# Kernel tuning notes

Hardware: AMD Instinct MI355X
Metric: run time of the kernel (lower is better)

The kernel has to match this reference:

```python
import jax, jax.numpy as jnp
import numpy as np

N_NODES = 100000
N_EDGES = 1600000
IN_DIM, HID_DIM, OUT_DIM = 128, 128, 64


def setup_inputs() -> dict:
    key = jax.random.key(0)
    k1, k2, k3, k4 = jax.random.split(key, 4)
    x = jax.random.normal(k1, (N_NODES, IN_DIM), dtype=jnp.float32)
    edge_index = jax.random.randint(k2, (2, N_EDGES), 0, N_NODES, dtype=jnp.int64)
    W1 = jax.random.normal(k3, (IN_DIM, HID_DIM), dtype=jnp.float32) * (1.0 / np.sqrt(IN_DIM))
    b1 = jnp.zeros((HID_DIM,), dtype=jnp.float32)
    W2 = jax.random.normal(k4, (HID_DIM, OUT_DIM), dtype=jnp.float32) * (1.0 / np.sqrt(HID_DIM))
    b2 = jnp.zeros((OUT_DIM,), dtype=jnp.float32)
    return {"x": x, "edge_index": edge_index, "W1": W1, "b1": b1, "W2": W2, "b2": b2}


def _gcn_conv(x, W, b, src, dst, num_nodes):
    # PyG GCNConv (normalize=True): h = D^{-1/2} A_hat D^{-1/2} (x W) + b
    h = x @ W  # [N, out]
    ones = jnp.ones(src.shape[0], dtype=h.dtype)
    deg = jax.ops.segment_sum(ones, dst, num_segments=num_nodes)  # in-degree incl self-loops
    dinv = jnp.where(deg > 0, jax.lax.rsqrt(deg), jnp.zeros_like(deg))
    norm = dinv[src] * dinv[dst]  # [E]
    msg = h[src] * norm[:, None]  # gather + scale, [E, out]
    out = jax.ops.segment_sum(msg, dst, num_segments=num_nodes)  # scatter-add
    return out + b


def reference(x, edge_index, W1, b1, W2, b2):
    n = x.shape[0]
    loop = jnp.arange(n, dtype=edge_index.dtype)
    src = jnp.concatenate([edge_index[0], loop])  # add_self_loops=True
    dst = jnp.concatenate([edge_index[1], loop])
    h = jax.nn.elu(_gcn_conv(x, W1, b1, src, dst, n))
    out = jax.nn.elu(_gcn_conv(h, W2, b2, src, dst, n))
    return out
```

## Files before the change

kernel.cpp:

```cpp
#include <hip/hip_runtime.h>
#include <hip/hip_bf16.h>

#define N_NODES 100000
#define N_EDGES 1600000
#define IN_DIM  128
#define HID_DIM 128
#define OUT_DIM 64

#define BKT_BITS 9
#define BKT_SIZE 512
#define NBUCK    ((N_NODES + BKT_SIZE - 1) / BKT_SIZE)
#define BCAP     8768
#define EPB      2048
#define CAST_BLKS 3125

typedef __attribute__((ext_vector_type(8))) short short8;
typedef __attribute__((ext_vector_type(4))) float floatx4;

__device__ __forceinline__ float eluf(float x) { return x > 0.0f ? x : expm1f(x); }
__device__ __forceinline__ unsigned short bfbits(float f) {
    union { __hip_bfloat16 h; unsigned short u; } c; c.h = __float2bfloat16(f); return c.u;
}
__device__ __forceinline__ unsigned packbf(float a, float b) {
    return (unsigned)bfbits(a) | ((unsigned)bfbits(b) << 16);
}
__device__ __forceinline__ float lo16(unsigned u) { return __uint_as_float(u << 16); }
__device__ __forceinline__ float hi16(unsigned u) { return __uint_as_float(u & 0xffff0000u); }

__device__ __forceinline__ int esrc(const int* ei, int e, int is64) {
    return is64 ? ei[2 * e] : ei[e];
}
__device__ __forceinline__ int edst(const int* ei, int e, int is64) {
    return is64 ? ei[2 * (N_EDGES + e)] : ei[N_EDGES + e];
}

__global__ void k_init(const int* __restrict__ ei, int* __restrict__ flag,
                       int* __restrict__ cursor) {
    __shared__ int acc;
    if (threadIdx.x == 0) acc = 0;
    __syncthreads();
    int v = 0;
    for (int e = threadIdx.x; e < 1024; e += 256) v |= ei[2 * e + 1];
    atomicOr(&acc, v);
    __syncthreads();
    if (threadIdx.x == 0) flag[0] = (acc == 0) ? 1 : 0;
    if (threadIdx.x < NBUCK) cursor[threadIdx.x] = 0;
}

__launch_bounds__(256)
__global__ void k_bucket(const int* __restrict__ ei, const int* __restrict__ flag,
                         int* __restrict__ cursor, unsigned* __restrict__ eb) {
    __shared__ int hist[NBUCK];
    __shared__ int base[NBUCK];
    int t = threadIdx.x;
    int is64 = flag[0];
    int e0 = blockIdx.x * EPB;
    int s[8], d[8];
#pragma unroll
    for (int q = 0; q < 8; q++) {
        int e = e0 + q * 256 + t;
        if (e < N_EDGES) { s[q] = esrc(ei, e, is64); d[q] = edst(ei, e, is64); }
        else d[q] = -1;
    }
    for (int i = t; i < NBUCK; i += 256) hist[i] = 0;
    __syncthreads();
#pragma unroll
    for (int q = 0; q < 8; q++)
        if (d[q] >= 0) atomicAdd(&hist[d[q] >> BKT_BITS], 1);
    __syncthreads();
    for (int i = t; i < NBUCK; i += 256) {
        int h = hist[i];
        base[i] = (h > 0) ? atomicAdd(&cursor[i], h) : 0;
    }
    __syncthreads();
#pragma unroll
    for (int q = 0; q < 8; q++)
        if (d[q] >= 0) {
            int bk = d[q] >> BKT_BITS;
            int p = atomicAdd(&base[bk], 1);
            if (p < BCAP)
                eb[bk * BCAP + p] = ((unsigned)s[q] << BKT_BITS) | (unsigned)(d[q] & (BKT_SIZE - 1));
        }
}

__launch_bounds__(256)
__global__ void k_csr_cast(const int* __restrict__ cursor, unsigned* __restrict__ eb,
                           unsigned short* __restrict__ row16, unsigned char* __restrict__ deg8,
                           float* __restrict__ dinv,
                           const float4* __restrict__ x4, uint2* __restrict__ xb) {
    __shared__ unsigned stage[BCAP];
    __shared__ int hist[BKT_SIZE];
    __shared__ int excl[BKT_SIZE];
    __shared__ int cur[BKT_SIZE];
    __shared__ int sc[256];
    int t = threadIdx.x, b = blockIdx.x;
    if (b >= NBUCK) {
        int i0 = (b - NBUCK) * 1024 + t;
#pragma unroll
        for (int q = 0; q < 4; q++) {
            int i = i0 + q * 256;
            if (i < N_NODES * (IN_DIM / 4)) {
                float4 v = x4[i];
                uint2 o = { packbf(v.x, v.y), packbf(v.z, v.w) };
                xb[i] = o;
            }
        }
        return;
    }
    int cbeg = b * BCAP;
    int count = cursor[b];
    if (count > BCAP) count = BCAP;
    for (int i = t; i < BKT_SIZE; i += 256) hist[i] = 0;
    __syncthreads();
    for (int i = t; i < count; i += 256) {
        unsigned e = eb[cbeg + i];
        stage[i] = e;
        atomicAdd(&hist[e & (BKT_SIZE - 1)], 1);
    }
    __syncthreads();
    int h0 = hist[2 * t], h1 = hist[2 * t + 1];
    int s = h0 + h1;
    sc[t] = s;
    __syncthreads();
    int acc = s;
    for (int off = 1; off < 256; off <<= 1) {
        int v = (t >= off) ? sc[t - off] : 0;
        __syncthreads();
        acc += v; sc[t] = acc;
        __syncthreads();
    }
    int ex = acc - s;
    excl[2 * t] = ex;       excl[2 * t + 1] = ex + h0;
    cur[2 * t] = ex;        cur[2 * t + 1] = ex + h0;
    int nbase = b * BKT_SIZE;
    for (int i = t; i < BKT_SIZE; i += 256) {
        int n = nbase + i;
        if (n < N_NODES) {
            row16[n] = (unsigned short)excl[i];
            deg8[n] = (unsigned char)hist[i];
            dinv[n] = rsqrtf((float)hist[i] + 1.0f);
        }
    }
    __syncthreads();
    for (int i = t; i < count; i += 256) {
        unsigned e = stage[i];
        int p = atomicAdd(&cur[e & (BKT_SIZE - 1)], 1);
        eb[cbeg + p] = e >> BKT_BITS;
    }
}

__launch_bounds__(256)
__global__ void k_gather1(const uint2* __restrict__ xb2, const float* __restrict__ dinv,
                          const unsigned short* __restrict__ row16,
                          const unsigned char* __restrict__ deg8,
                          const unsigned* __restrict__ csr, uint2* __restrict__ agg2) {
    int w = (blockIdx.x * blockDim.x + threadIdx.x) >> 5;
    int p = threadIdx.x & 31;
    if (w >= N_NODES) return;
    int beg = (w >> BKT_BITS) * BCAP + row16[w];
    int end = beg + deg8[w];
    float dd = dinv[w];
    uint2 sv = xb2[w * 32 + p];
    float a0 = lo16(sv.x) * dd, a1 = hi16(sv.x) * dd;
    float a2 = lo16(sv.y) * dd, a3 = hi16(sv.y) * dd;
    int j = beg;
    for (; j + 8 <= end; j += 8) {
        int s[8]; float wd[8]; uint2 u[8];
#pragma unroll
        for (int q = 0; q < 8; q++) s[q] = (int)csr[j + q];
#pragma unroll
        for (int q = 0; q < 8; q++) wd[q] = dinv[s[q]];
#pragma unroll
        for (int q = 0; q < 8; q++) u[q] = xb2[s[q] * 32 + p];
#pragma unroll
        for (int q = 0; q < 8; q++) {
            a0 += lo16(u[q].x) * wd[q]; a1 += hi16(u[q].x) * wd[q];
            a2 += lo16(u[q].y) * wd[q]; a3 += hi16(u[q].y) * wd[q];
        }
    }
    for (; j + 2 <= end; j += 2) {
        int s0 = (int)csr[j], s1 = (int)csr[j + 1];
        float w0 = dinv[s0], w1 = dinv[s1];
        uint2 u0 = xb2[s0 * 32 + p];
        uint2 u1 = xb2[s1 * 32 + p];
        a0 += lo16(u0.x) * w0 + lo16(u1.x) * w1; a1 += hi16(u0.x) * w0 + hi16(u1.x) * w1;
        a2 += lo16(u0.y) * w0 + lo16(u1.y) * w1; a3 += hi16(u0.y) * w0 + hi16(u1.y) * w1;
    }
    if (j < end) {
        int s0 = (int)csr[j]; float w0 = dinv[s0];
        uint2 u0 = xb2[s0 * 32 + p];
        a0 += lo16(u0.x) * w0; a1 += hi16(u0.x) * w0;
        a2 += lo16(u0.y) * w0; a3 += hi16(u0.y) * w0;
    }
    uint2 o = { packbf(a0 * dd, a1 * dd), packbf(a2 * dd, a3 * dd) };
    agg2[w * 32 + p] = o;
}

__launch_bounds__(256)
__global__ void k_gather2(const uint2* __restrict__ h2, const float* __restrict__ dinv,
                          const unsigned short* __restrict__ row16,
                          const unsigned char* __restrict__ deg8,
                          const unsigned* __restrict__ csr,
                          const float* __restrict__ b2, float4* __restrict__ out) {
    int w = (blockIdx.x * blockDim.x + threadIdx.x) >> 4;
    int p = threadIdx.x & 15;
    if (w >= N_NODES) return;
    float4 bias = *(const float4*)(b2 + 4 * p);
    int beg = (w >> BKT_BITS) * BCAP + row16[w];
    int end = beg + deg8[w];
    float dd = dinv[w];
    uint2 sv = h2[w * 16 + p];
    float a0 = lo16(sv.x) * dd, a1 = hi16(sv.x) * dd;
    float a2 = lo16(sv.y) * dd, a3 = hi16(sv.y) * dd;
    int j = beg;
    for (; j + 8 <= end; j += 8) {
        int s[8]; float wd[8]; uint2 u[8];
#pragma unroll
        for (int q = 0; q < 8; q++) s[q] = (int)csr[j + q];
#pragma unroll
        for (int q = 0; q < 8; q++) wd[q] = dinv[s[q]];
#pragma unroll
        for (int q = 0; q < 8; q++) u[q] = h2[s[q] * 16 + p];
#pragma unroll
        for (int q = 0; q < 8; q++) {
            a0 += lo16(u[q].x) * wd[q]; a1 += hi16(u[q].x) * wd[q];
            a2 += lo16(u[q].y) * wd[q]; a3 += hi16(u[q].y) * wd[q];
        }
    }
    for (; j + 2 <= end; j += 2) {
        int s0 = (int)csr[j], s1 = (int)csr[j + 1];
        float w0 = dinv[s0], w1 = dinv[s1];
        uint2 u0 = h2[s0 * 16 + p];
        uint2 u1 = h2[s1 * 16 + p];
        a0 += lo16(u0.x) * w0 + lo16(u1.x) * w1; a1 += hi16(u0.x) * w0 + hi16(u1.x) * w1;
        a2 += lo16(u0.y) * w0 + lo16(u1.y) * w1; a3 += hi16(u0.y) * w0 + hi16(u1.y) * w1;
    }
    if (j < end) {
        int s0 = (int)csr[j]; float w0 = dinv[s0];
        uint2 u0 = h2[s0 * 16 + p];
        a0 += lo16(u0.x) * w0; a1 += hi16(u0.x) * w0;
        a2 += lo16(u0.y) * w0; a3 += hi16(u0.y) * w0;
    }
    a0 *= dd; a1 *= dd; a2 *= dd; a3 *= dd;
    float4 r = { eluf(a0 + bias.x), eluf(a1 + bias.y), eluf(a2 + bias.z), eluf(a3 + bias.w) };
    out[w * 16 + p] = r;
}

__launch_bounds__(256)
__global__ void k_gemm1_mfma(unsigned* __restrict__ agg, const float* __restrict__ W1,
                             const float* __restrict__ b1, int nblk) {
    __shared__ short w1p[4][8][64][8];
    int t = threadIdx.x;
    for (int idx = t; idx < 8192; idx += 256) {
        int j2 = idx & 3, l = (idx >> 2) & 63, ct = (idx >> 8) & 7, kk = idx >> 11;
        int k = kk * 32 + (l >> 4) * 8 + j2 * 2;
        int c = ct * 16 + (l & 15);
        ((unsigned*)w1p)[idx] = packbf(W1[k * HID_DIM + c], W1[(k + 1) * HID_DIM + c]);
    }
    int lane = t & 63, wave = t >> 6;
    int q = lane >> 4, m = lane & 15;
    floatx4 bias[8];
#pragma unroll
    for (int ct = 0; ct < 8; ct++) bias[ct] = *(const floatx4*)(b1 + ct * 16 + q * 4);
    __syncthreads();
    for (int blk = blockIdx.x * 4 + wave; blk < nblk; blk += gridDim.x * 4) {
        int r = blk * 16 + m;
        const short8* arow = (const short8*)(agg + r * 64);
        short8 bfr[4];
#pragma unroll
        for (int kk = 0; kk < 4; kk++) bfr[kk] = arow[kk * 4 + q];
        floatx4 acc[8];
#pragma unroll
        for (int ct = 0; ct < 8; ct++) acc[ct] = (floatx4)0.0f;
#pragma unroll
        for (int kk = 0; kk < 4; kk++)
#pragma unroll
            for (int ct = 0; ct < 8; ct++) {
                short8 af = *(const short8*)(&w1p[kk][ct][lane][0]);
                acc[ct] = __builtin_amdgcn_mfma_f32_16x16x32_bf16(af, bfr[kk], acc[ct], 0, 0, 0);
            }
        unsigned* hrow = agg + r * 64;
#pragma unroll
        for (int ct = 0; ct < 8; ct++) {
            uint2 o;
            o.x = packbf(eluf(acc[ct][0] + bias[ct][0]), eluf(acc[ct][1] + bias[ct][1]));
            o.y = packbf(eluf(acc[ct][2] + bias[ct][2]), eluf(acc[ct][3] + bias[ct][3]));
            *(uint2*)(hrow + ct * 8 + q * 2) = o;
        }
    }
}

__launch_bounds__(256)
__global__ void k_gemm2_mfma(const unsigned* __restrict__ h1, const float* __restrict__ W2,
                             unsigned* __restrict__ h2, int nblk) {
    __shared__ short w2p[4][4][64][8];
    int t = threadIdx.x;
    for (int idx = t; idx < 4096; idx += 256) {
        int j2 = idx & 3, l = (idx >> 2) & 63, ct = (idx >> 8) & 3, kk = idx >> 10;
        int k = kk * 32 + (l >> 4) * 8 + j2 * 2;
        int c = ct * 16 + (l & 15);
        ((unsigned*)w2p)[idx] = packbf(W2[k * OUT_DIM + c], W2[(k + 1) * OUT_DIM + c]);
    }
    int lane = t & 63, wave = t >> 6;
    int q = lane >> 4, m = lane & 15;
    __syncthreads();
    for (int blk = blockIdx.x * 4 + wave; blk < nblk; blk += gridDim.x * 4) {
        int r = blk * 16 + m;
        const short8* arow = (const short8*)(h1 + r * 64);
        short8 bfr[4];
#pragma unroll
        for (int kk = 0; kk < 4; kk++) bfr[kk] = arow[kk * 4 + q];
        floatx4 acc[4];
#pragma unroll
        for (int ct = 0; ct < 4; ct++) acc[ct] = (floatx4)0.0f;
#pragma unroll
        for (int kk = 0; kk < 4; kk++)
#pragma unroll
            for (int ct = 0; ct < 4; ct++) {
                short8 af = *(const short8*)(&w2p[kk][ct][lane][0]);
                acc[ct] = __builtin_amdgcn_mfma_f32_16x16x32_bf16(af, bfr[kk], acc[ct], 0, 0, 0);
            }
        unsigned* orow = h2 + r * 32;
#pragma unroll
        for (int ct = 0; ct < 4; ct++) {
            uint2 o;
            o.x = packbf(acc[ct][0], acc[ct][1]);
            o.y = packbf(acc[ct][2], acc[ct][3]);
            *(uint2*)(orow + ct * 8 + q * 2) = o;
        }
    }
}

extern "C" void kernel_launch(void* const* d_in, const int* in_sizes, int n_in,
                              void* d_out, int out_size, void* d_ws, size_t ws_size,
                              hipStream_t stream) {
    const float* x  = (const float*)d_in[0];
    const int*   ei = (const int*)d_in[1];
    const float* W1 = (const float*)d_in[2];
    const float* b1 = (const float*)d_in[3];
    const float* W2 = (const float*)d_in[4];
    const float* b2 = (const float*)d_in[5];

    const size_t OFF_FLAG  = 0;
    const size_t OFF_CUR   = 16;
    const size_t OFF_ROW16 = 272;
    const size_t OFF_DEG8  = 50272;
    const size_t OFF_DINV  = 75272;
    const size_t OFF_EB    = 175272;
    const size_t OFF_XB    = 1893800;
    const size_t OFF_AGG   = 8293800;
    const size_t needed = (OFF_AGG + 6400000) * 4;
    if (ws_size < needed) return;

    int*            flag   = (int*)d_ws + OFF_FLAG;
    int*            cursor = (int*)d_ws + OFF_CUR;
    unsigned short* row16  = (unsigned short*)((int*)d_ws + OFF_ROW16);
    unsigned char*  deg8   = (unsigned char*)((int*)d_ws + OFF_DEG8);
    float*          dinv   = (float*)d_ws + OFF_DINV;
    unsigned*       eb     = (unsigned*)d_ws + OFF_EB;
    unsigned*       xb     = (unsigned*)d_ws + OFF_XB;
    unsigned*       agg    = (unsigned*)d_ws + OFF_AGG;

    k_init<<<1, 256, 0, stream>>>(ei, flag, cursor);
    k_bucket<<<(N_EDGES + EPB - 1) / EPB, 256, 0, stream>>>(ei, flag, cursor, eb);
    k_csr_cast<<<NBUCK + CAST_BLKS, 256, 0, stream>>>(cursor, eb, row16, deg8, dinv,
                                                      (const float4*)x, (uint2*)xb);

    k_gather1<<<(N_NODES * 32 + 255) / 256, 256, 0, stream>>>(
        (const uint2*)xb, dinv, row16, deg8, eb, (uint2*)agg);
    k_gemm1_mfma<<<1024, 256, 0, stream>>>(agg, W1, b1, N_NODES / 16);

    k_gemm2_mfma<<<1024, 256, 0, stream>>>(agg, W2, xb, N_NODES / 16);
    k_gather2<<<(N_NODES * 16 + 255) / 256, 256, 0, stream>>>(
        (const uint2*)xb, dinv, row16, deg8, eb, b2, (float4*)d_out);
}
```

Before: 326.9 us.

## Pre-scale features by dinv, tile-sort CSR neighbors, widen gathers to full wave

Source rows are multiplied by dinv once, in a separate cast kernel for layer 1 and in the GEMM2 epilogue for layer 2. This removes the per-edge dinv lookup and multiply from both gathers. The CSR build now sorts each node's neighbors by source tile (8 tiles), which should make gathered rows more local in cache. Both gathers use one 64-lane wave per node with readfirstlane bounds, and layer 2 splits edges across two half-waves combined with a shuffle. In exchange, the input cast is no longer fused into the CSR kernel, so it runs as an extra serialized launch, and CSR binning uses more shared memory.

```diff
diff --git a/kernel.cpp b/kernel.cpp
--- a/kernel.cpp
+++ b/kernel.cpp
@@ -12,7 +12,7 @@
 #define NBUCK    ((N_NODES + BKT_SIZE - 1) / BKT_SIZE)
 #define BCAP     8768
 #define EPB      2048
-#define CAST_BLKS 3125
+#define NTILE    8
 
 typedef __attribute__((ext_vector_type(8))) short short8;
 typedef __attribute__((ext_vector_type(4))) float floatx4;
@@ -26,6 +26,7 @@
 }
 __device__ __forceinline__ float lo16(unsigned u) { return __uint_as_float(u << 16); }
 __device__ __forceinline__ float hi16(unsigned u) { return __uint_as_float(u & 0xffff0000u); }
+__device__ __forceinline__ unsigned tile_of(unsigned src) { return (src * 8u) / 100000u; }
 
 __device__ __forceinline__ int esrc(const int* ei, int e, int is64) {
     return is64 ? ei[2 * e] : ei[e];
@@ -84,42 +85,29 @@
 }
 
 __launch_bounds__(256)
-__global__ void k_csr_cast(const int* __restrict__ cursor, unsigned* __restrict__ eb,
-                           unsigned short* __restrict__ row16, unsigned char* __restrict__ deg8,
-                           float* __restrict__ dinv,
-                           const float4* __restrict__ x4, uint2* __restrict__ xb) {
+__global__ void k_csr(const int* __restrict__ cursor, unsigned* __restrict__ eb,
+                      unsigned short* __restrict__ row16, unsigned char* __restrict__ deg8,
+                      float* __restrict__ dinv) {
     __shared__ unsigned stage[BCAP];
-    __shared__ int hist[BKT_SIZE];
-    __shared__ int excl[BKT_SIZE];
-    __shared__ int cur[BKT_SIZE];
+    __shared__ int bins[BKT_SIZE * NTILE];
     __shared__ int sc[256];
     int t = threadIdx.x, b = blockIdx.x;
-    if (b >= NBUCK) {
-        int i0 = (b - NBUCK) * 1024 + t;
-#pragma unroll
-        for (int q = 0; q < 4; q++) {
-            int i = i0 + q * 256;
-            if (i < N_NODES * (IN_DIM / 4)) {
-                float4 v = x4[i];
-                uint2 o = { packbf(v.x, v.y), packbf(v.z, v.w) };
-                xb[i] = o;
-            }
-        }
-        return;
-    }
     int cbeg = b * BCAP;
     int count = cursor[b];
     if (count > BCAP) count = BCAP;
-    for (int i = t; i < BKT_SIZE; i += 256) hist[i] = 0;
+    for (int i = t; i < BKT_SIZE * NTILE; i += 256) bins[i] = 0;
     __syncthreads();
     for (int i = t; i < count; i += 256) {
         unsigned e = eb[cbeg + i];
         stage[i] = e;
-        atomicAdd(&hist[e & (BKT_SIZE - 1)], 1);
-    }
-    __syncthreads();
-    int h0 = hist[2 * t], h1 = hist[2 * t + 1];
-    int s = h0 + h1;
+        unsigned key = ((e & (BKT_SIZE - 1)) << 3) + tile_of(e >> BKT_BITS);
+        atomicAdd(&bins[key], 1);
+    }
+    __syncthreads();
+    int loc[16];
+    int s = 0;
+#pragma unroll
+    for (int i = 0; i < 16; i++) { loc[i] = bins[t * 16 + i]; s += loc[i]; }
     sc[t] = s;
     __syncthreads();
     int acc = s;
@@ -129,121 +117,143 @@
         acc += v; sc[t] = acc;
         __syncthreads();
     }
-    int ex = acc - s;
-    excl[2 * t] = ex;       excl[2 * t + 1] = ex + h0;
-    cur[2 * t] = ex;        cur[2 * t + 1] = ex + h0;
+    int run = acc - s;
+#pragma unroll
+    for (int i = 0; i < 16; i++) { bins[t * 16 + i] = run; run += loc[i]; }
+    __syncthreads();
     int nbase = b * BKT_SIZE;
     for (int i = t; i < BKT_SIZE; i += 256) {
         int n = nbase + i;
         if (n < N_NODES) {
-            row16[n] = (unsigned short)excl[i];
-            deg8[n] = (unsigned char)hist[i];
-            dinv[n] = rsqrtf((float)hist[i] + 1.0f);
+            int st = bins[i << 3];
+            int en = (i == BKT_SIZE - 1) ? count : bins[(i + 1) << 3];
+            row16[n] = (unsigned short)st;
+            deg8[n] = (unsigned char)(en - st);
+            dinv[n] = rsqrtf((float)(en - st) + 1.0f);
         }
     }
     __syncthreads();
     for (int i = t; i < count; i += 256) {
         unsigned e = stage[i];
-        int p = atomicAdd(&cur[e & (BKT_SIZE - 1)], 1);
-        eb[cbeg + p] = e >> BKT_BITS;
-    }
-}
-
-__launch_bounds__(256)
-__global__ void k_gather1(const uint2* __restrict__ xb2, const float* __restrict__ dinv,
+        unsigned src = e >> BKT_BITS;
+        unsigned key = ((e & (BKT_SIZE - 1)) << 3) + tile_of(src);
+        int p = atomicAdd(&bins[key], 1);
+        eb[cbeg + p] = src;
+    }
+}
+
+__global__ void k_cast_scale(const float4* __restrict__ x4, const float* __restrict__ dinv,
+                             uint2* __restrict__ xbs) {
+    int i = blockIdx.x * blockDim.x + threadIdx.x;
+    if (i >= N_NODES * (IN_DIM / 4)) return;
+    float dd = dinv[i >> 5];
+    float4 v = x4[i];
+    uint2 o = { packbf(v.x * dd, v.y * dd), packbf(v.z * dd, v.w * dd) };
+    xbs[i] = o;
+}
+
+__launch_bounds__(256)
+__global__ void k_gather1(const unsigned* __restrict__ xbs, const float* __restrict__ dinv,
                           const unsigned short* __restrict__ row16,
                           const unsigned char* __restrict__ deg8,
-                          const unsigned* __restrict__ csr, uint2* __restrict__ agg2) {
-    int w = (blockIdx.x * blockDim.x + threadIdx.x) >> 5;
-    int p = threadIdx.x & 31;
+                          const unsigned* __restrict__ csr, unsigned* __restrict__ agg) {
+    int w = (blockIdx.x * blockDim.x + threadIdx.x) >> 6;
+    int lane = threadIdx.x & 63;
     if (w >= N_NODES) return;
     int beg = (w >> BKT_BITS) * BCAP + row16[w];
-    int end = beg + deg8[w];
+    int dg = deg8[w];
+    beg = __builtin_amdgcn_readfirstlane(beg);
+    int end = beg + __builtin_amdgcn_readfirstlane(dg);
     float dd = dinv[w];
-    uint2 sv = xb2[w * 32 + p];
-    float a0 = lo16(sv.x) * dd, a1 = hi16(sv.x) * dd;
-    float a2 = lo16(sv.y) * dd, a3 = hi16(sv.y) * dd;
+    unsigned sv = xbs[w * 64 + lane];
+    float a0 = lo16(sv), a1 = hi16(sv);
     int j = beg;
     for (; j + 8 <= end; j += 8) {
-        int s[8]; float wd[8]; uint2 u[8];
+        int s[8]; unsigned u[8];
 #pragma unroll
         for (int q = 0; q < 8; q++) s[q] = (int)csr[j + q];
 #pragma unroll
-        for (int q = 0; q < 8; q++) wd[q] = dinv[s[q]];
-#pragma unroll
-        for (int q = 0; q < 8; q++) u[q] = xb2[s[q] * 32 + p];
-#pragma unroll
-        for (int q = 0; q < 8; q++) {
-            a0 += lo16(u[q].x) * wd[q]; a1 += hi16(u[q].x) * wd[q];
-            a2 += lo16(u[q].y) * wd[q]; a3 += hi16(u[q].y) * wd[q];
-        }
-    }
-    for (; j + 2 <= end; j += 2) {
+        for (int q = 0; q < 8; q++) u[q] = xbs[s[q] * 64 + lane];
+#pragma unroll
+        for (int q = 0; q < 8; q++) { a0 += lo16(u[q]); a1 += hi16(u[q]); }
+    }
+    if (j + 4 <= end) {
+        int s[4]; unsigned u[4];
+#pragma unroll
+        for (int q = 0; q < 4; q++) s[q] = (int)csr[j + q];
+#pragma unroll
+        for (int q = 0; q < 4; q++) u[q] = xbs[s[q] * 64 + lane];
+#pragma unroll
+        for (int q = 0; q < 4; q++) { a0 += lo16(u[q]); a1 += hi16(u[q]); }
+        j += 4;
+    }
+    if (j + 2 <= end) {
         int s0 = (int)csr[j], s1 = (int)csr[j + 1];
-        float w0 = dinv[s0], w1 = dinv[s1];
-        uint2 u0 = xb2[s0 * 32 + p];
-        uint2 u1 = xb2[s1 * 32 + p];
-        a0 += lo16(u0.x) * w0 + lo16(u1.x) * w1; a1 += hi16(u0.x) * w0 + hi16(u1.x) * w1;
-        a2 += lo16(u0.y) * w0 + lo16(u1.y) * w1; a3 += hi16(u0.y) * w0 + hi16(u1.y) * w1;
+        unsigned u0 = xbs[s0 * 64 + lane], u1 = xbs[s1 * 64 + lane];
+        a0 += lo16(u0) + lo16(u1); a1 += hi16(u0) + hi16(u1);
+        j += 2;
     }
     if (j < end) {
-        int s0 = (int)csr[j]; float w0 = dinv[s0];
-        uint2 u0 = xb2[s0 * 32 + p];
-        a0 += lo16(u0.x) * w0; a1 += hi16(u0.x) * w0;
-        a2 += lo16(u0.y) * w0; a3 += hi16(u0.y) * w0;
-    }
-    uint2 o = { packbf(a0 * dd, a1 * dd), packbf(a2 * dd, a3 * dd) };
-    agg2[w * 32 + p] = o;
-}
-
-__launch_bounds__(256)
-__global__ void k_gather2(const uint2* __restrict__ h2, const float* __restrict__ dinv,
+        unsigned u0 = xbs[(int)csr[j] * 64 + lane];
+        a0 += lo16(u0); a1 += hi16(u0);
+    }
+    agg[w * 64 + lane] = packbf(a0 * dd, a1 * dd);
+}
+
+__launch_bounds__(256)
+__global__ void k_gather2(const unsigned* __restrict__ h2s, const float* __restrict__ dinv,
                           const unsigned short* __restrict__ row16,
                           const unsigned char* __restrict__ deg8,
                           const unsigned* __restrict__ csr,
-                          const float* __restrict__ b2, float4* __restrict__ out) {
-    int w = (blockIdx.x * blockDim.x + threadIdx.x) >> 4;
-    int p = threadIdx.x & 15;
+                          const float* __restrict__ b2, float2* __restrict__ out) {
+    int w = (blockIdx.x * blockDim.x + threadIdx.x) >> 6;
+    int lane = threadIdx.x & 63;
     if (w >= N_NODES) return;
-    float4 bias = *(const float4*)(b2 + 4 * p);
+    int half = lane >> 5, p = lane & 31;
     int beg = (w >> BKT_BITS) * BCAP + row16[w];
-    int end = beg + deg8[w];
+    int dg = deg8[w];
+    beg = __builtin_amdgcn_readfirstlane(beg);
+    int end = beg + __builtin_amdgcn_readfirstlane(dg);
     float dd = dinv[w];
-    uint2 sv = h2[w * 16 + p];
-    float a0 = lo16(sv.x) * dd, a1 = hi16(sv.x) * dd;
-    float a2 = lo16(sv.y) * dd, a3 = hi16(sv.y) * dd;
+    unsigned sv = h2s[w * 32 + p];
+    float a0 = half ? 0.0f : lo16(sv);
+    float a1 = half ? 0.0f : hi16(sv);
     int j = beg;
     for (; j + 8 <= end; j += 8) {
-        int s[8]; float wd[8]; uint2 u[8];
+        int s[8]; unsigned u[4];
 #pragma unroll
         for (int q = 0; q < 8; q++) s[q] = (int)csr[j + q];
 #pragma unroll
-        for (int q = 0; q < 8; q++) wd[q] = dinv[s[q]];
-#pragma unroll
-        for (int q = 0; q < 8; q++) u[q] = h2[s[q] * 16 + p];
-#pragma unroll
-        for (int q = 0; q < 8; q++) {
-            a0 += lo16(u[q].x) * wd[q]; a1 += hi16(u[q].x) * wd[q];
-            a2 += lo16(u[q].y) * wd[q]; a3 += hi16(u[q].y) * wd[q];
-        }
-    }
-    for (; j + 2 <= end; j += 2) {
+        for (int i = 0; i < 4; i++) u[i] = h2s[s[2 * i + half] * 32 + p];
+#pragma unroll
+        for (int i = 0; i < 4; i++) { a0 += lo16(u[i]); a1 += hi16(u[i]); }
+    }
+    if (j + 4 <= end) {
+        int s[4];
+#pragma unroll
+        for (int q = 0; q < 4; q++) s[q] = (int)csr[j + q];
+        unsigned u0 = h2s[s[half] * 32 + p];
+        unsigned u1 = h2s[s[2 + half] * 32 + p];
+        a0 += lo16(u0) + lo16(u1); a1 += hi16(u0) + hi16(u1);
+        j += 4;
+    }
+    if (j + 2 <= end) {
         int s0 = (int)csr[j], s1 = (int)csr[j + 1];
-        float w0 = dinv[s0], w1 = dinv[s1];
-        uint2 u0 = h2[s0 * 16 + p];
-        uint2 u1 = h2[s1 * 16 + p];
-        a0 += lo16(u0.x) * w0 + lo16(u1.x) * w1; a1 += hi16(u0.x) * w0 + hi16(u1.x) * w1;
-        a2 += lo16(u0.y) * w0 + lo16(u1.y) * w1; a3 += hi16(u0.y) * w0 + hi16(u1.y) * w1;
-    }
-    if (j < end) {
-        int s0 = (int)csr[j]; float w0 = dinv[s0];
-        uint2 u0 = h2[s0 * 16 + p];
-        a0 += lo16(u0.x) * w0; a1 += hi16(u0.x) * w0;
-        a2 += lo16(u0.y) * w0; a3 += hi16(u0.y) * w0;
-    }
-    a0 *= dd; a1 *= dd; a2 *= dd; a3 *= dd;
-    float4 r = { eluf(a0 + bias.x), eluf(a1 + bias.y), eluf(a2 + bias.z), eluf(a3 + bias.w) };
-    out[w * 16 + p] = r;
+        unsigned u = h2s[(half ? s1 : s0) * 32 + p];
+        a0 += lo16(u); a1 += hi16(u);
+        j += 2;
+    }
+    if (j < end && !half) {
+        unsigned u = h2s[(int)csr[j] * 32 + p];
+        a0 += lo16(u); a1 += hi16(u);
+    }
+    a0 += __shfl_xor(a0, 32);
+    a1 += __shfl_xor(a1, 32);
+    if (!half) {
+        float2 bias = *(const float2*)(b2 + 2 * p);
+        float2 r = { eluf(a0 * dd + bias.x), eluf(a1 * dd + bias.y) };
+        out[w * 32 + p] = r;
+    }
 }
 
 __launch_bounds__(256)
@@ -292,7 +302,8 @@
 
 __launch_bounds__(256)
 __global__ void k_gemm2_mfma(const unsigned* __restrict__ h1, const float* __restrict__ W2,
-                             unsigned* __restrict__ h2, int nblk) {
+                             const float* __restrict__ dinv, unsigned* __restrict__ h2s,
+                             int nblk) {
     __shared__ short w2p[4][4][64][8];
     int t = threadIdx.x;
     for (int idx = t; idx < 4096; idx += 256) {
@@ -320,12 +331,13 @@
                 short8 af = *(const short8*)(&w2p[kk][ct][lane][0]);
                 acc[ct] = __builtin_amdgcn_mfma_f32_16x16x32_bf16(af, bfr[kk], acc[ct], 0, 0, 0);
             }
-        unsigned* orow = h2 + r * 32;
+        float ddr = dinv[r];
+        unsigned* orow = h2s + r * 32;
 #pragma unroll
         for (int ct = 0; ct < 4; ct++) {
             uint2 o;
-            o.x = packbf(acc[ct][0], acc[ct][1]);
-            o.y = packbf(acc[ct][2], acc[ct][3]);
+            o.x = packbf(acc[ct][0] * ddr, acc[ct][1] * ddr);
+            o.y = packbf(acc[ct][2] * ddr, acc[ct][3] * ddr);
             *(uint2*)(orow + ct * 8 + q * 2) = o;
         }
     }
@@ -358,19 +370,21 @@
     unsigned char*  deg8   = (unsigned char*)((int*)d_ws + OFF_DEG8);
     float*          dinv   = (float*)d_ws + OFF_DINV;
     unsigned*       eb     = (unsigned*)d_ws + OFF_EB;
-    unsigned*       xb     = (unsigned*)d_ws + OFF_XB;
+    unsigned*       xbs    = (unsigned*)d_ws + OFF_XB;
     unsigned*       agg    = (unsigned*)d_ws + OFF_AGG;
 
     k_init<<<1, 256, 0, stream>>>(ei, flag, cursor);
     k_bucket<<<(N_EDGES + EPB - 1) / EPB, 256, 0, stream>>>(ei, flag, cursor, eb);
-    k_csr_cast<<<NBUCK + CAST_BLKS, 256, 0, stream>>>(cursor, eb, row16, deg8, dinv,
-                                                      (const float4*)x, (uint2*)xb);
-
-    k_gather1<<<(N_NODES * 32 + 255) / 256, 256, 0, stream>>>(
-        (const uint2*)xb, dinv, row16, deg8, eb, (uint2*)agg);
+    k_csr<<<NBUCK, 256, 0, stream>>>(cursor, eb, row16, deg8, dinv);
+
+    k_cast_scale<<<(N_NODES * (IN_DIM / 4) + 255) / 256, 256, 0, stream>>>(
+        (const float4*)x, dinv, (uint2*)xbs);
+
+    k_gather1<<<(N_NODES * 64 + 255) / 256, 256, 0, stream>>>(
+        xbs, dinv, row16, deg8, eb, agg);
     k_gemm1_mfma<<<1024, 256, 0, stream>>>(agg, W1, b1, N_NODES / 16);
 
-    k_gemm2_mfma<<<1024, 256, 0, stream>>>(agg, W2, xb, N_NODES / 16);
-    k_gather2<<<(N_NODES * 16 + 255) / 256, 256, 0, stream>>>(
-        (const uint2*)xb, dinv, row16, deg8, eb, b2, (float4*)d_out);
-}
+    k_gemm2_mfma<<<1024, 256, 0, stream>>>(agg, W2, dinv, xbs, N_NODES / 16);
+    k_gather2<<<(N_NODES * 64 + 255) / 256, 256, 0, stream>>>(
+        xbs, dinv, row16, deg8, eb, b2, (float2*)d_out);
+}
```

Result: no change. 327.2 us (+0.1%).
